# Optimization experiments

Measured on AMD Instinct MI355X. Metric: run time of the kernel, lower is better.

Reference implementation:

```python
import jax, jax.numpy as jnp
import numpy as np

# shift search range (matches init_kwargs)
MIN_SX, MAX_SX = -4, 4
MIN_SY, MAX_SY = -4, 4
B, C, H, W = 4, 3, 512, 512


def _shift(x, sx, sy):
    """torch.roll on dims (1,2) of a [C,H,W] tensor, zeroing wrapped rows/cols.

    Equivalent to AutomatedShiftFix.shift: positive sx zeros rows [:sx],
    negative sx zeros rows [sx:]; same for sy on the W axis.
    """
    h, w = x.shape[1], x.shape[2]
    shifted = jnp.roll(x, (sx, sy), axis=(1, 2))
    i = jnp.arange(h)[:, None]   # [H,1]
    j = jnp.arange(w)[None, :]   # [1,W]
    mask_h = jnp.where(sx >= 0, i >= sx, i < h + sx)
    mask_w = jnp.where(sy >= 0, j >= sy, j < w + sy)
    mask = (mask_h & mask_w).astype(x.dtype)  # [H,W]
    return shifted * mask[None]


def _all_shifts():
    sx = jnp.arange(MIN_SX, MAX_SX + 1)
    sy = jnp.arange(MIN_SY, MAX_SY + 1)
    # outer loop over shift_x, inner over shift_y -> 'ij' matches torch ordering
    return jnp.stack(jnp.meshgrid(sx, sy, indexing="ij"), axis=-1).reshape(-1, 2)  # [Ns,2]


def setup_inputs() -> dict:
    key = jax.random.key(0)
    k1, k2 = jax.random.split(key)
    x_ref = jax.random.normal(k1, (B, C, H, W), dtype=jnp.float32)
    x = jax.random.normal(k2, (B, C, H, W), dtype=jnp.float32)
    return {"x_ref": x_ref, "x": x}


def reference(x_ref, x):
    shifts = _all_shifts()  # [Ns,2] int32

    def sims_one(xr, xi):  # xr, xi: [C,H,W]
        # similarity for every candidate shift: sum over (C,H,W) of shifted*ref
        return jax.vmap(lambda s: jnp.sum(_shift(xi, s[0], s[1]) * xr))(shifts)  # [Ns]

    sims = jax.vmap(sims_one)(x_ref, x)          # [B, Ns]
    best = jnp.argmax(sims, axis=1)              # [B]
    best_shifts = shifts[best]                   # [B, 2]
    out = jax.vmap(lambda xi, s: _shift(xi, s[0], s[1]))(x, best_shifts)  # [B,C,H,W]
    return out, best_shifts
```

## Files before the change

kernel.cpp:

```cpp
#include <hip/hip_runtime.h>

#define BB 4
#define CC 3
#define HH 512
#define WW 512
#define NS 81
#define IMG (HH * WW)
#define CHW (CC * IMG)
#define STRIP 32
#define NSTRIP (HH / STRIP)
#define NBLK (BB * CC * NSTRIP * 9)

#define BEST_OFF (NBLK * 9 * sizeof(float))

#define C4(v, i) ((i) == 0 ? (v).x : (i) == 1 ? (v).y : (i) == 2 ? (v).z : (v).w)

__global__ __launch_bounds__(256, 4) void k_sims(const float* __restrict__ xref,
                                                 const float* __restrict__ x,
                                                 float* __restrict__ partials) {
    int bid  = blockIdx.x;
    int sxi  = bid % 9;
    int tmp  = bid / 9;
    int strip = tmp % NSTRIP;
    int bc   = tmp / NSTRIP;
    const float* xp = x    + (size_t)bc * IMG;
    const float* rp = xref + (size_t)bc * IMG;
    int tid  = threadIdx.x;
    int lane = tid & 63;
    int wave = tid >> 6;
    int j0   = lane << 3;
    int sx   = sxi - 4;
    int ip0  = strip * STRIP + wave * 8;

    float acc[9];
#pragma unroll
    for (int s = 0; s < 9; ++s) acc[s] = 0.f;

#pragma unroll
    for (int rr = 0; rr < 8; ++rr) {
        int ip = ip0 + rr;
        int ii = ip + sx;
        if ((unsigned)ii >= HH) continue;

        const float* xrow = xp + ip * WW + j0;
        const float* rrow = rp + ii * WW + j0;
        float4 xa = *(const float4*)(xrow);
        float4 xb = *(const float4*)(xrow + 4);
        float4 ra = *(const float4*)(rrow);
        float4 rb = *(const float4*)(rrow + 4);

        float p0 = __shfl_up(rb.x, 1, 64);
        float p1 = __shfl_up(rb.y, 1, 64);
        float p2 = __shfl_up(rb.z, 1, 64);
        float p3 = __shfl_up(rb.w, 1, 64);
        if (lane == 0) { p0 = p1 = p2 = p3 = 0.f; }
        float n0 = __shfl_down(ra.x, 1, 64);
        float n1 = __shfl_down(ra.y, 1, 64);
        float n2 = __shfl_down(ra.z, 1, 64);
        float n3 = __shfl_down(ra.w, 1, 64);
        if (lane == 63) { n0 = n1 = n2 = n3 = 0.f; }

#define P4(i) ((i) == 0 ? p0 : (i) == 1 ? p1 : (i) == 2 ? p2 : p3)
#define N4(i) ((i) == 0 ? n0 : (i) == 1 ? n1 : (i) == 2 ? n2 : n3)
#pragma unroll
        for (int syi = 0; syi < 9; ++syi) {
#pragma unroll
            for (int k = 0; k < 8; ++k) {
                int i = k + syi;
                float wv = (i < 4)  ? P4(i)
                         : (i < 8)  ? C4(ra, i - 4)
                         : (i < 12) ? C4(rb, i - 8)
                         :            N4(i - 12);
                float xv = (k < 4) ? C4(xa, k) : C4(xb, k - 4);
                acc[syi] += xv * wv;
            }
        }
#undef P4
#undef N4
    }

    __shared__ float part[4][9];
#pragma unroll
    for (int s = 0; s < 9; ++s) {
        float v = acc[s];
        for (int off = 32; off; off >>= 1) v += __shfl_down(v, off, 64);
        if (lane == 0) part[wave][s] = v;
    }
    __syncthreads();
    if (tid < 9)
        partials[bid * 9 + tid] = part[0][tid] + part[1][tid]
                                + part[2][tid] + part[3][tid];
}

__global__ __launch_bounds__(512) void k_argmax(const float* __restrict__ partials,
                                                int* __restrict__ best,
                                                float* __restrict__ outTail) {
    int b = blockIdx.x;
    int t = threadIdx.x;
    __shared__ double lds[486];
    __shared__ double vals[NS];
    if (t < 486) {
        int slot = t / 6;
        int sub  = t % 6;
        int sxi = slot / 9, syi = slot % 9;
        double acc = 0.0;
#pragma unroll
        for (int k = 0; k < 8; ++k) {
            int q  = sub * 8 + k;
            int c  = q >> 4;
            int st = q & 15;
            int pb = ((b * CC + c) * NSTRIP + st) * 9 + sxi;
            acc += (double)partials[pb * 9 + syi];
        }
        lds[t] = acc;
    }
    __syncthreads();
    if (t < NS) {
        double s = 0.0;
#pragma unroll
        for (int k = 0; k < 6; ++k) s += lds[t * 6 + k];
        vals[t] = s;
    }
    __syncthreads();
    if (t == 0) {
        double bv = vals[0];
        int bi = 0;
        for (int s = 1; s < NS; ++s)
            if (vals[s] > bv) { bv = vals[s]; bi = s; }
        int sx = bi / 9 - 4;
        int sy = bi % 9 - 4;
        best[b * 2]     = sx;
        best[b * 2 + 1] = sy;
        outTail[b * 2]     = (float)sx;
        outTail[b * 2 + 1] = (float)sy;
    }
}

__global__ __launch_bounds__(256) void k_apply(const float* __restrict__ x,
                                               const int* __restrict__ best,
                                               float* __restrict__ out) {
    int blk = blockIdx.x;
    int bc  = blk >> 8;
    int tid = threadIdx.x;
    int row = ((blk & 255) << 1) + (tid >> 7);
    int j0  = (tid & 127) << 2;
    int b   = bc / CC;
    int sx  = best[b * 2];
    int sy  = best[b * 2 + 1];
    int is  = row - sx;
    float4 v = make_float4(0.f, 0.f, 0.f, 0.f);
    if ((unsigned)is < HH) {
        const float* src = x + (size_t)bc * IMG + is * WW;
        int js0 = j0 - sy;
        if (js0 >= 0 && js0 + 3 < WW) {
            v = *(const float4*)(src + js0);
        } else {
            float* vv = (float*)&v;
#pragma unroll
            for (int k = 0; k < 4; ++k) {
                int js = js0 + k;
                if ((unsigned)js < WW) vv[k] = src[js];
            }
        }
    }
    *(float4*)(out + (size_t)bc * IMG + row * WW + j0) = v;
}

extern "C" void kernel_launch(void* const* d_in, const int* in_sizes, int n_in,
                              void* d_out, int out_size, void* d_ws, size_t ws_size,
                              hipStream_t stream) {
    const float* xref = (const float*)d_in[0];
    const float* x    = (const float*)d_in[1];
    float* out = (float*)d_out;

    float* partials = (float*)d_ws;
    int*   best     = (int*)((char*)d_ws + BEST_OFF);

    k_sims<<<NBLK, 256, 0, stream>>>(xref, x, partials);

    k_argmax<<<BB, 512, 0, stream>>>(partials, best, out + (size_t)BB * CHW);

    int applyBlocks = (BB * CC * HH) / 2;
    k_apply<<<applyBlocks, 256, 0, stream>>>(x, best, out);
}
```

Measured before the change: 109.2 us.

## Fold argmax into apply kernel via double atomics into per-batch sim buffer

The separate argmax kernel is removed. Each sims block now atomically adds its double-precision partial sums straight into a per-batch 81-entry similarity buffer, which is zeroed by a memset first. Every apply block then reloads the 81 sims for its batch and redoes the argmax with a wave reduction before copying. This drops one kernel launch and the partials round trip, but adds a memset, contended fp64 atomics and a redundant argmax in each of the 3072 apply blocks. The order of the atomic adds is not fixed, so an argmax tie could resolve differently from run to run.

After: 108.4 us (median of 2 runs). No clear change (-0.7%).

```diff
diff --git a/kernel.cpp b/kernel.cpp
--- a/kernel.cpp
+++ b/kernel.cpp
@@ -11,18 +11,18 @@
 #define NSTRIP (HH / STRIP)
 #define NBLK (BB * CC * NSTRIP * 9)
 
-#define BEST_OFF (NBLK * 9 * sizeof(float))
 
 #define C4(v, i) ((i) == 0 ? (v).x : (i) == 1 ? (v).y : (i) == 2 ? (v).z : (v).w)
 
 __global__ __launch_bounds__(256, 4) void k_sims(const float* __restrict__ xref,
                                                  const float* __restrict__ x,
-                                                 float* __restrict__ partials) {
+                                                 double* __restrict__ sims) {
     int bid  = blockIdx.x;
     int sxi  = bid % 9;
     int tmp  = bid / 9;
     int strip = tmp % NSTRIP;
     int bc   = tmp / NSTRIP;
+    int b    = bc / CC;
     const float* xp = x    + (size_t)bc * IMG;
     const float* rp = xref + (size_t)bc * IMG;
     int tid  = threadIdx.x;
@@ -87,66 +87,51 @@
         if (lane == 0) part[wave][s] = v;
     }
     __syncthreads();
-    if (tid < 9)
-        partials[bid * 9 + tid] = part[0][tid] + part[1][tid]
-                                + part[2][tid] + part[3][tid];
-}
-
-__global__ __launch_bounds__(512) void k_argmax(const float* __restrict__ partials,
-                                                int* __restrict__ best,
-                                                float* __restrict__ outTail) {
-    int b = blockIdx.x;
-    int t = threadIdx.x;
-    __shared__ double lds[486];
-    __shared__ double vals[NS];
-    if (t < 486) {
-        int slot = t / 6;
-        int sub  = t % 6;
-        int sxi = slot / 9, syi = slot % 9;
-        double acc = 0.0;
-#pragma unroll
-        for (int k = 0; k < 8; ++k) {
-            int q  = sub * 8 + k;
-            int c  = q >> 4;
-            int st = q & 15;
-            int pb = ((b * CC + c) * NSTRIP + st) * 9 + sxi;
-            acc += (double)partials[pb * 9 + syi];
-        }
-        lds[t] = acc;
-    }
-    __syncthreads();
-    if (t < NS) {
-        double s = 0.0;
-#pragma unroll
-        for (int k = 0; k < 6; ++k) s += lds[t * 6 + k];
-        vals[t] = s;
-    }
-    __syncthreads();
-    if (t == 0) {
-        double bv = vals[0];
-        int bi = 0;
-        for (int s = 1; s < NS; ++s)
-            if (vals[s] > bv) { bv = vals[s]; bi = s; }
-        int sx = bi / 9 - 4;
-        int sy = bi % 9 - 4;
-        best[b * 2]     = sx;
-        best[b * 2 + 1] = sy;
-        outTail[b * 2]     = (float)sx;
-        outTail[b * 2 + 1] = (float)sy;
+    if (tid < 9) {
+        double tot = (double)part[0][tid] + (double)part[1][tid]
+                   + (double)part[2][tid] + (double)part[3][tid];
+        atomicAdd(&sims[b * NS + sxi * 9 + tid], tot);
     }
 }
 
 __global__ __launch_bounds__(256) void k_apply(const float* __restrict__ x,
-                                               const int* __restrict__ best,
-                                               float* __restrict__ out) {
+                                               const double* __restrict__ sims,
+                                               float* __restrict__ out,
+                                               float* __restrict__ outTail) {
     int blk = blockIdx.x;
     int bc  = blk >> 8;
     int tid = threadIdx.x;
+    int b   = bc / CC;
+
+    __shared__ double vals[NS];
+    __shared__ int bestIdx;
+    if (tid < NS) vals[tid] = sims[b * NS + tid];
+    __syncthreads();
+    if (tid < 64) {
+        double v = vals[tid];
+        int    i = tid;
+        if (tid < NS - 64) {
+            double v2 = vals[tid + 64];
+            if (v2 > v) { v = v2; i = tid + 64; }
+        }
+        for (int off = 32; off; off >>= 1) {
+            double ov = __shfl_down(v, off, 64);
+            int    oi = __shfl_down(i, off, 64);
+            if (ov > v || (ov == v && oi < i)) { v = ov; i = oi; }
+        }
+        if (tid == 0) bestIdx = i;
+    }
+    __syncthreads();
+    int bi = bestIdx;
+    int sx = bi / 9 - 4;
+    int sy = bi % 9 - 4;
+    if (blk == ((b * CC) << 8) && tid == 0) {
+        outTail[b * 2]     = (float)sx;
+        outTail[b * 2 + 1] = (float)sy;
+    }
+
     int row = ((blk & 255) << 1) + (tid >> 7);
     int j0  = (tid & 127) << 2;
-    int b   = bc / CC;
-    int sx  = best[b * 2];
-    int sy  = best[b * 2 + 1];
     int is  = row - sx;
     float4 v = make_float4(0.f, 0.f, 0.f, 0.f);
     if ((unsigned)is < HH) {
@@ -173,13 +158,12 @@
     const float* x    = (const float*)d_in[1];
     float* out = (float*)d_out;
 
-    float* partials = (float*)d_ws;
-    int*   best     = (int*)((char*)d_ws + BEST_OFF);
+    double* sims = (double*)d_ws;
 
-    k_sims<<<NBLK, 256, 0, stream>>>(xref, x, partials);
+    hipMemsetAsync(sims, 0, BB * NS * sizeof(double), stream);
 
-    k_argmax<<<BB, 512, 0, stream>>>(partials, best, out + (size_t)BB * CHW);
+    k_sims<<<NBLK, 256, 0, stream>>>(xref, x, sims);
 
     int applyBlocks = (BB * CC * HH) / 2;
-    k_apply<<<applyBlocks, 256, 0, stream>>>(x, best, out);
+    k_apply<<<applyBlocks, 256, 0, stream>>>(x, sims, out, out + (size_t)BB * CHW);
 }
```
